# Optimization experiments

Measured on AMD Instinct MI355X. Metric: run time of the kernel, lower is better.

Reference implementation:

```python
import jax, jax.numpy as jnp
import numpy as np

IN_F = 4096
OUT_F = 4096
RANK = 16
ALPHA = 16
SCALING = ALPHA / RANK  # 1.0


def setup_inputs() -> dict:
    key = jax.random.key(0)
    k_x, k_w, k_b, k_a = jax.random.split(key, 4)
    x = jax.random.normal(k_x, (4, 2048, IN_F), dtype=jnp.float32)
    # frozen base linear params
    W = jax.random.normal(k_w, (OUT_F, IN_F), dtype=jnp.float32) * (1.0 / np.sqrt(IN_F))
    b = jax.random.normal(k_b, (OUT_F,), dtype=jnp.float32) * 0.01
    # LoRA params: A kaiming-uniform-like, B zeros per initial_weights(); use small
    bound = np.sqrt(6.0 / IN_F)  # kaiming_uniform(a=sqrt(5)) bound approx
    lora_A = jax.random.uniform(k_a, (RANK, IN_F), dtype=jnp.float32, minval=-bound, maxval=bound)
    lora_B = jax.random.normal(jax.random.fold_in(key, 7), (OUT_F, RANK), dtype=jnp.float32) * 0.01
    lora_bias = jnp.zeros((OUT_F,), dtype=jnp.float32)
    return {"x": x, "W": W, "b": b, "lora_A": lora_A, "lora_B": lora_B, "lora_bias": lora_bias}


def reference(x, W, b, lora_A, lora_B, lora_bias):
    # Original: F.linear(x, W + scaling*B@A, bias=b + lora_bias); dropout is Identity (p=0).
    # Algebraically equivalent form avoiding the [out,in] delta materialization:
    # y = x@W^T + scaling * (x@A^T)@B^T + (b + lora_bias)
    base = jnp.einsum('bsi,oi->bso', x, W)
    low = jnp.einsum('bsr,or->bso', jnp.einsum('bsi,ri->bsr', x, lora_A), lora_B)
    return base + SCALING * low + (b + lora_bias)
```

## Files before the change

kernel.cpp:

```cpp
#include <hip/hip_runtime.h>
#include <hip/hip_bf16.h>
#include <stdint.h>


#define M_DIM 8192
#define N_DIM 4096
#define K_DIM 4096
#define NT    (K_DIM / 64)

typedef __attribute__((ext_vector_type(8))) short bf16x8;
typedef __attribute__((ext_vector_type(4))) float f32x4;

#define BARRIER() __builtin_amdgcn_s_barrier()
#define WAITV8() asm volatile("s_waitcnt vmcnt(8)" ::: "memory")
#define WAITV4() asm volatile("s_waitcnt vmcnt(4)" ::: "memory")
#define WAITV0() asm volatile("s_waitcnt vmcnt(0)" ::: "memory")

static __device__ __forceinline__ unsigned short f2bf(float f) {
    unsigned int u = __builtin_bit_cast(unsigned int, f);
    unsigned int r = (u + 0x7fffu + ((u >> 16) & 1u)) >> 16;
    return (unsigned short)r;
}

__global__ __launch_bounds__(256) void conv_x_kernel(
    const float* __restrict__ x, unsigned short* __restrict__ xb) {
    size_t i = ((size_t)blockIdx.x * 256 + threadIdx.x) * 8;
    float4 a = *(const float4*)(x + i);
    float4 c = *(const float4*)(x + i + 4);
    union { unsigned short us[8]; uint4 v; } u;
    u.us[0] = f2bf(a.x); u.us[1] = f2bf(a.y); u.us[2] = f2bf(a.z); u.us[3] = f2bf(a.w);
    u.us[4] = f2bf(c.x); u.us[5] = f2bf(c.y); u.us[6] = f2bf(c.z); u.us[7] = f2bf(c.w);
    *(uint4*)(xb + i) = u.v;
}

__global__ __launch_bounds__(512) void conv_w_kernel(
    const float* __restrict__ W, const float* __restrict__ lA,
    const float* __restrict__ lB, unsigned short* __restrict__ Wb) {
    const int nb = blockIdx.x * 4;
    const int k0 = threadIdx.x * 8;

    float acc[4][8];
#pragma unroll
    for (int r = 0; r < 4; ++r) {
        const float4* w4 = (const float4*)(W + (size_t)(nb + r) * K_DIM + k0);
        float4 v0 = w4[0], v1 = w4[1];
        acc[r][0] = v0.x; acc[r][1] = v0.y; acc[r][2] = v0.z; acc[r][3] = v0.w;
        acc[r][4] = v1.x; acc[r][5] = v1.y; acc[r][6] = v1.z; acc[r][7] = v1.w;
    }
    float brs[4][16];
#pragma unroll
    for (int r = 0; r < 4; ++r)
#pragma unroll
        for (int t = 0; t < 16; ++t) brs[r][t] = lB[(size_t)(nb + r) * 16 + t];

#pragma unroll
    for (int t = 0; t < 16; ++t) {
        const float4* a4 = (const float4*)(lA + (size_t)t * K_DIM + k0);
        float4 v0 = a4[0], v1 = a4[1];
        float av[8] = {v0.x, v0.y, v0.z, v0.w, v1.x, v1.y, v1.z, v1.w};
#pragma unroll
        for (int r = 0; r < 4; ++r)
#pragma unroll
            for (int j = 0; j < 8; ++j) acc[r][j] += brs[r][t] * av[j];
    }
#pragma unroll
    for (int r = 0; r < 4; ++r) {
        union { unsigned short us[8]; uint4 v; } u;
#pragma unroll
        for (int j = 0; j < 8; ++j) u.us[j] = f2bf(acc[r][j]);
        *(uint4*)(Wb + (size_t)(nb + r) * K_DIM + k0) = u.v;
    }
}

__global__ __launch_bounds__(512, 2) void gemm_kernel(
    const unsigned short* __restrict__ A,
    const unsigned short* __restrict__ B,
    const float* __restrict__ bvec, const float* __restrict__ lbvec,
    float* __restrict__ C) {
    const int tid = threadIdx.x;
    const int lane = tid & 63;
    const int wid = tid >> 6;
    const int wr = wid >> 2;
    const int wc = wid & 3;

    const int bid = blockIdx.x;
    const int ntile = (bid & 7) * 2 + ((bid >> 3) & 1);
    const int mtile = bid >> 4;
    const int m0 = mtile * 256, n0 = ntile * 256;

    __shared__ __align__(16) unsigned short ldsA[2 * 2 * 128 * 64];
    __shared__ __align__(16) unsigned short ldsB[2 * 2 * 128 * 64];

    const int lr8 = lane >> 3;
    const int cch = (lane & 7) ^ lr8;
    const unsigned short* aSb = A + (size_t)(m0 + lr8) * K_DIM + cch * 8;
    const unsigned short* bSb = B + (size_t)(n0 + lr8) * K_DIM + cch * 8;

    auto stageA = [&](int par_, int h, int kt) {
#pragma unroll
        for (int s = 0; s < 2; ++s) {
            const int j = wid * 2 + s;
            const unsigned short* g = aSb + (size_t)(h * 128 + j * 8) * K_DIM + kt * 64;
            __builtin_amdgcn_global_load_lds(
                (const __attribute__((address_space(1))) void*)g,
                (__attribute__((address_space(3))) void*)(ldsA + (par_ * 2 + h) * 8192 + j * 512),
                16, 0, 0);
        }
    };
    auto stageB = [&](int par_, int h, int kt) {
#pragma unroll
        for (int s = 0; s < 2; ++s) {
            const int j = wid * 2 + s;
            const unsigned short* g = bSb + (size_t)(h * 128 + j * 8) * K_DIM + kt * 64;
            __builtin_amdgcn_global_load_lds(
                (const __attribute__((address_space(1))) void*)g,
                (__attribute__((address_space(3))) void*)(ldsB + (par_ * 2 + h) * 8192 + j * 512),
                16, 0, 0);
        }
    };

    const int rowByte = (lane & 15) * 128;
    const int swz = (lane & 7) << 4;
    const int kc0 = (0 * 64 + (lane >> 4) * 16) ^ swz;
    const int kc1 = (1 * 64 + (lane >> 4) * 16) ^ swz;
    const int baseBoff = (wc & 1) * 4096;

    auto readA = [&](int par_, int mf, int kk) -> bf16x8 {
        const char* p = (const char*)(ldsA + (par_ * 2 + wr) * 8192 + mf * 1024) +
                        rowByte + (kk ? kc1 : kc0);
        return *(const bf16x8*)p;
    };
    auto readB = [&](int par_, int nf, int kk) -> bf16x8 {
        const char* p = (const char*)(ldsB + (par_ * 2 + (wc >> 1)) * 8192 + baseBoff + nf * 1024) +
                        rowByte + (kk ? kc1 : kc0);
        return *(const bf16x8*)p;
    };

    f32x4 acc[8][4] = {};
    bf16x8 a[4][2], b[4][2];

    auto mfmaQ = [&](int qm, int qn) {
#pragma unroll
        for (int i = 0; i < 4; ++i)
#pragma unroll
            for (int jn = 0; jn < 2; ++jn)
#pragma unroll
                for (int kk = 0; kk < 2; ++kk)
                    acc[qm * 4 + i][qn * 2 + jn] = __builtin_amdgcn_mfma_f32_16x16x32_bf16(
                        a[i][kk], b[qn * 2 + jn][kk], acc[qm * 4 + i][qn * 2 + jn], 0, 0, 0);
    };

    stageB(0, 0, 0); stageB(0, 1, 0); stageA(0, 0, 0); stageA(0, 1, 0);
    stageB(1, 0, 1); stageB(1, 1, 1); stageA(1, 0, 1); stageA(1, 1, 1);
    WAITV8();
    BARRIER();
#pragma unroll
    for (int nf = 0; nf < 2; ++nf)
#pragma unroll
        for (int kk = 0; kk < 2; ++kk) b[nf][kk] = readB(0, nf, kk);

#define KTILE(kt, par)                                                          \
    {                                                                           \
                         \
        _Pragma("unroll") for (int i = 0; i < 4; ++i)                           \
            _Pragma("unroll") for (int kk = 0; kk < 2; ++kk)                    \
                a[i][kk] = readA(par, i, kk);                                    \
        BARRIER();                                                              \
        __builtin_amdgcn_s_setprio(1); mfmaQ(0, 0); __builtin_amdgcn_s_setprio(0); \
        BARRIER();                                                              \
                                                \
        _Pragma("unroll") for (int nf = 2; nf < 4; ++nf)                        \
            _Pragma("unroll") for (int kk = 0; kk < 2; ++kk)                    \
                b[nf][kk] = readB(par, nf, kk);                                  \
        BARRIER();                                                              \
        __builtin_amdgcn_s_setprio(1); mfmaQ(0, 1); __builtin_amdgcn_s_setprio(0); \
        BARRIER();                                                              \
                                             \
        _Pragma("unroll") for (int i = 0; i < 4; ++i)                           \
            _Pragma("unroll") for (int kk = 0; kk < 2; ++kk)                    \
                a[i][kk] = readA(par, 4 + i, kk);                                \
        if ((kt) + 2 < NT) { stageB(par, 0, (kt) + 2); stageB(par, 1, (kt) + 2); WAITV4(); } \
        else { WAITV0(); }                                                      \
        BARRIER();                                                              \
        __builtin_amdgcn_s_setprio(1); mfmaQ(1, 0); __builtin_amdgcn_s_setprio(0); \
        BARRIER();                                                              \
         \
        if ((kt) + 2 < NT) { stageA(par, 0, (kt) + 2); stageA(par, 1, (kt) + 2); } \
        if ((kt) + 1 < NT) {                                                    \
            _Pragma("unroll") for (int nf = 0; nf < 2; ++nf)                    \
                _Pragma("unroll") for (int kk = 0; kk < 2; ++kk)                \
                    b[nf][kk] = readB((par) ^ 1, nf, kk);                        \
        }                                                                       \
        BARRIER();                                                              \
        __builtin_amdgcn_s_setprio(1); mfmaQ(1, 1); __builtin_amdgcn_s_setprio(0); \
        BARRIER();                                                              \
    }

#pragma unroll 1
    for (int kt = 0; kt < NT; kt += 2) {
        KTILE(kt, 0);
        KTILE(kt + 1, 1);
    }
#undef KTILE

#pragma unroll
    for (int nf = 0; nf < 4; ++nf) {
        const int gc = n0 + wc * 64 + nf * 16 + (lane & 15);
        const float bv = bvec[gc] + lbvec[gc];
#pragma unroll
        for (int mf = 0; mf < 8; ++mf) {
            const int gr0 = m0 + wr * 128 + mf * 16 + (lane >> 4) * 4;
            f32x4 v = acc[mf][nf];
#pragma unroll
            for (int j = 0; j < 4; ++j)
                __builtin_nontemporal_store(v[j] + bv, &C[(size_t)(gr0 + j) * N_DIM + gc]);
        }
    }
}

__global__ __launch_bounds__(256) void naive_kernel(
    const float* __restrict__ x, const float* __restrict__ W,
    const float* __restrict__ b, const float* __restrict__ lA,
    const float* __restrict__ lB, const float* __restrict__ lb,
    float* __restrict__ out) {
    __shared__ float xs[K_DIM];
    __shared__ float ts[16];
    const int m = blockIdx.x;
    const int tid = threadIdx.x;
    for (int k = tid; k < K_DIM; k += 256) xs[k] = x[(size_t)m * K_DIM + k];
    if (tid < 16) ts[tid] = 0.f;
    __syncthreads();
    float part[16] = {};
    for (int k = tid * 16; k < tid * 16 + 16; ++k) {
        float xv = xs[k];
#pragma unroll
        for (int r = 0; r < 16; ++r) part[r] += xv * lA[(size_t)r * K_DIM + k];
    }
#pragma unroll
    for (int r = 0; r < 16; ++r) atomicAdd(&ts[r], part[r]);
    __syncthreads();
    const int n = blockIdx.y * 256 + tid;
    float acc = b[n] + lb[n];
#pragma unroll
    for (int r = 0; r < 16; ++r) acc += ts[r] * lB[(size_t)n * 16 + r];
    const float* wrow = W + (size_t)n * K_DIM;
    for (int k = 0; k < K_DIM; ++k) acc += xs[k] * wrow[k];
    out[(size_t)m * N_DIM + n] = acc;
}

extern "C" void kernel_launch(void* const* d_in, const int* in_sizes, int n_in,
                              void* d_out, int out_size, void* d_ws, size_t ws_size,
                              hipStream_t stream) {
    const float* x  = (const float*)d_in[0];
    const float* W  = (const float*)d_in[1];
    const float* b  = (const float*)d_in[2];
    const float* lA = (const float*)d_in[3];
    const float* lB = (const float*)d_in[4];
    const float* lb = (const float*)d_in[5];
    float* out = (float*)d_out;

    const size_t xb_bytes = (size_t)M_DIM * K_DIM * 2;
    const size_t wb_bytes = (size_t)N_DIM * K_DIM * 2;

    if (ws_size >= xb_bytes + wb_bytes) {
        unsigned short* xb = (unsigned short*)d_ws;
        unsigned short* wb = (unsigned short*)((char*)d_ws + xb_bytes);

        conv_x_kernel<<<(M_DIM * K_DIM) / (256 * 8), 256, 0, stream>>>(x, xb);
        conv_w_kernel<<<N_DIM / 4, 512, 0, stream>>>(W, lA, lB, wb);

        gemm_kernel<<<(M_DIM / 256) * (N_DIM / 256), 512, 0, stream>>>(xb, wb, b, lb, out);
    } else {
        dim3 grid(M_DIM, N_DIM / 256);
        naive_kernel<<<grid, 256, 0, stream>>>(x, W, b, lA, lB, lb, out);
    }
}
```

Measured before the change: 322.3 us.

## Restructure GEMM k-tile loop to k-major MFMA order with fewer barriers

```diff
diff --git a/kernel.cpp b/kernel.cpp
--- a/kernel.cpp
+++ b/kernel.cpp
@@ -13,7 +13,6 @@
 
 #define BARRIER() __builtin_amdgcn_s_barrier()
 #define WAITV8() asm volatile("s_waitcnt vmcnt(8)" ::: "memory")
-#define WAITV4() asm volatile("s_waitcnt vmcnt(4)" ::: "memory")
 #define WAITV0() asm volatile("s_waitcnt vmcnt(0)" ::: "memory")
 
 static __device__ __forceinline__ unsigned short f2bf(float f) {
@@ -137,62 +136,51 @@
     };
 
     f32x4 acc[8][4] = {};
-    bf16x8 a[4][2], b[4][2];
-
-    auto mfmaQ = [&](int qm, int qn) {
-#pragma unroll
-        for (int i = 0; i < 4; ++i)
-#pragma unroll
-            for (int jn = 0; jn < 2; ++jn)
-#pragma unroll
-                for (int kk = 0; kk < 2; ++kk)
-                    acc[qm * 4 + i][qn * 2 + jn] = __builtin_amdgcn_mfma_f32_16x16x32_bf16(
-                        a[i][kk], b[qn * 2 + jn][kk], acc[qm * 4 + i][qn * 2 + jn], 0, 0, 0);
-    };
+    bf16x8 A_[4], B0_[4], B1_[4];
 
     stageB(0, 0, 0); stageB(0, 1, 0); stageA(0, 0, 0); stageA(0, 1, 0);
     stageB(1, 0, 1); stageB(1, 1, 1); stageA(1, 0, 1); stageA(1, 1, 1);
     WAITV8();
     BARRIER();
-#pragma unroll
-    for (int nf = 0; nf < 2; ++nf)
-#pragma unroll
-        for (int kk = 0; kk < 2; ++kk) b[nf][kk] = readB(0, nf, kk);
 
 #define KTILE(kt, par)                                                          \
     {                                                                           \
-                         \
-        _Pragma("unroll") for (int i = 0; i < 4; ++i)                           \
-            _Pragma("unroll") for (int kk = 0; kk < 2; ++kk)                    \
-                a[i][kk] = readA(par, i, kk);                                    \
+        _Pragma("unroll") for (int i = 0; i < 4; ++i) A_[i] = readA(par, i, 0); \
+        _Pragma("unroll") for (int j = 0; j < 4; ++j) B0_[j] = readB(par, j, 0);\
+        _Pragma("unroll") for (int j = 0; j < 4; ++j) B1_[j] = readB(par, j, 1);\
+        __builtin_amdgcn_s_setprio(1);                                          \
+        _Pragma("unroll") for (int i = 0; i < 4; ++i)                           \
+            _Pragma("unroll") for (int j = 0; j < 4; ++j)                       \
+                acc[i][j] = __builtin_amdgcn_mfma_f32_16x16x32_bf16(            \
+                    A_[i], B0_[j], acc[i][j], 0, 0, 0);                         \
+        __builtin_amdgcn_s_setprio(0);                                          \
+        _Pragma("unroll") for (int i = 0; i < 4; ++i) A_[i] = readA(par, 4 + i, 0); \
+        __builtin_amdgcn_s_setprio(1);                                          \
+        _Pragma("unroll") for (int i = 0; i < 4; ++i)                           \
+            _Pragma("unroll") for (int j = 0; j < 4; ++j)                       \
+                acc[4 + i][j] = __builtin_amdgcn_mfma_f32_16x16x32_bf16(        \
+                    A_[i], B0_[j], acc[4 + i][j], 0, 0, 0);                     \
+        __builtin_amdgcn_s_setprio(0);                                          \
+        _Pragma("unroll") for (int i = 0; i < 4; ++i) A_[i] = readA(par, i, 1); \
+        __builtin_amdgcn_s_setprio(1);                                          \
+        _Pragma("unroll") for (int i = 0; i < 4; ++i)                           \
+            _Pragma("unroll") for (int j = 0; j < 4; ++j)                       \
+                acc[i][j] = __builtin_amdgcn_mfma_f32_16x16x32_bf16(            \
+                    A_[i], B1_[j], acc[i][j], 0, 0, 0);                         \
+        __builtin_amdgcn_s_setprio(0);                                          \
+        _Pragma("unroll") for (int i = 0; i < 4; ++i) A_[i] = readA(par, 4 + i, 1); \
+        __builtin_amdgcn_s_setprio(1);                                          \
+        _Pragma("unroll") for (int i = 0; i < 4; ++i)                           \
+            _Pragma("unroll") for (int j = 0; j < 4; ++j)                       \
+                acc[4 + i][j] = __builtin_amdgcn_mfma_f32_16x16x32_bf16(        \
+                    A_[i], B1_[j], acc[4 + i][j], 0, 0, 0);                     \
+        __builtin_amdgcn_s_setprio(0);                                          \
         BARRIER();                                                              \
-        __builtin_amdgcn_s_setprio(1); mfmaQ(0, 0); __builtin_amdgcn_s_setprio(0); \
-        BARRIER();                                                              \
-                                                \
-        _Pragma("unroll") for (int nf = 2; nf < 4; ++nf)                        \
-            _Pragma("unroll") for (int kk = 0; kk < 2; ++kk)                    \
-                b[nf][kk] = readB(par, nf, kk);                                  \
-        BARRIER();                                                              \
-        __builtin_amdgcn_s_setprio(1); mfmaQ(0, 1); __builtin_amdgcn_s_setprio(0); \
-        BARRIER();                                                              \
-                                             \
-        _Pragma("unroll") for (int i = 0; i < 4; ++i)                           \
-            _Pragma("unroll") for (int kk = 0; kk < 2; ++kk)                    \
-                a[i][kk] = readA(par, 4 + i, kk);                                \
-        if ((kt) + 2 < NT) { stageB(par, 0, (kt) + 2); stageB(par, 1, (kt) + 2); WAITV4(); } \
-        else { WAITV0(); }                                                      \
-        BARRIER();                                                              \
-        __builtin_amdgcn_s_setprio(1); mfmaQ(1, 0); __builtin_amdgcn_s_setprio(0); \
-        BARRIER();                                                              \
-         \
-        if ((kt) + 2 < NT) { stageA(par, 0, (kt) + 2); stageA(par, 1, (kt) + 2); } \
-        if ((kt) + 1 < NT) {                                                    \
-            _Pragma("unroll") for (int nf = 0; nf < 2; ++nf)                    \
-                _Pragma("unroll") for (int kk = 0; kk < 2; ++kk)                \
-                    b[nf][kk] = readB((par) ^ 1, nf, kk);                        \
-        }                                                                       \
-        BARRIER();                                                              \
-        __builtin_amdgcn_s_setprio(1); mfmaQ(1, 1); __builtin_amdgcn_s_setprio(0); \
+        if ((kt) + 2 < NT) {                                                    \
+            stageB(par, 0, (kt) + 2); stageB(par, 1, (kt) + 2);                 \
+            stageA(par, 0, (kt) + 2); stageA(par, 1, (kt) + 2);                 \
+            WAITV8();                                                           \
+        } else { WAITV0(); }                                                    \
         BARRIER();                                                              \
     }
 
```

New measurement: 330.2 us. +2.5%, slower.

## Restructure GEMM to 4 waves with 128x128 warp tiles and k-half register double-buffering

Applied to the files above, without the earlier changes.

```diff
diff --git a/kernel.cpp b/kernel.cpp
--- a/kernel.cpp
+++ b/kernel.cpp
@@ -12,9 +12,11 @@
 typedef __attribute__((ext_vector_type(4))) float f32x4;
 
 #define BARRIER() __builtin_amdgcn_s_barrier()
-#define WAITV8() asm volatile("s_waitcnt vmcnt(8)" ::: "memory")
-#define WAITV4() asm volatile("s_waitcnt vmcnt(4)" ::: "memory")
-#define WAITV0() asm volatile("s_waitcnt vmcnt(0)" ::: "memory")
+#define WAITV16() asm volatile("s_waitcnt vmcnt(16)" ::: "memory")
+#define WAITV0()  asm volatile("s_waitcnt vmcnt(0)" ::: "memory")
+#define LGKM0()   do { asm volatile("s_waitcnt lgkmcnt(0)" ::: "memory"); \
+                       __builtin_amdgcn_sched_barrier(0); } while (0)
+#define SCHED_FENCE() __builtin_amdgcn_sched_barrier(0)
 
 static __device__ __forceinline__ unsigned short f2bf(float f) {
     unsigned int u = __builtin_bit_cast(unsigned int, f);
@@ -72,7 +74,7 @@
     }
 }
 
-__global__ __launch_bounds__(512, 2) void gemm_kernel(
+__global__ __launch_bounds__(256, 1) void gemm_kernel(
     const unsigned short* __restrict__ A,
     const unsigned short* __restrict__ B,
     const float* __restrict__ bvec, const float* __restrict__ lbvec,
@@ -80,8 +82,8 @@
     const int tid = threadIdx.x;
     const int lane = tid & 63;
     const int wid = tid >> 6;
-    const int wr = wid >> 2;
-    const int wc = wid & 3;
+    const int wr = wid >> 1;
+    const int wc = wid & 1;
 
     const int bid = blockIdx.x;
     const int ntile = (bid & 7) * 2 + ((bid >> 3) & 1);
@@ -98,8 +100,8 @@
 
     auto stageA = [&](int par_, int h, int kt) {
 #pragma unroll
-        for (int s = 0; s < 2; ++s) {
-            const int j = wid * 2 + s;
+        for (int s = 0; s < 4; ++s) {
+            const int j = wid * 4 + s;
             const unsigned short* g = aSb + (size_t)(h * 128 + j * 8) * K_DIM + kt * 64;
             __builtin_amdgcn_global_load_lds(
                 (const __attribute__((address_space(1))) void*)g,
@@ -109,8 +111,8 @@
     };
     auto stageB = [&](int par_, int h, int kt) {
 #pragma unroll
-        for (int s = 0; s < 2; ++s) {
-            const int j = wid * 2 + s;
+        for (int s = 0; s < 4; ++s) {
+            const int j = wid * 4 + s;
             const unsigned short* g = bSb + (size_t)(h * 128 + j * 8) * K_DIM + kt * 64;
             __builtin_amdgcn_global_load_lds(
                 (const __attribute__((address_space(1))) void*)g,
@@ -118,12 +120,15 @@
                 16, 0, 0);
         }
     };
+    auto stageTile = [&](int par_, int kt) {
+        stageB(par_, 0, kt); stageB(par_, 1, kt);
+        stageA(par_, 0, kt); stageA(par_, 1, kt);
+    };
 
     const int rowByte = (lane & 15) * 128;
     const int swz = (lane & 7) << 4;
     const int kc0 = (0 * 64 + (lane >> 4) * 16) ^ swz;
     const int kc1 = (1 * 64 + (lane >> 4) * 16) ^ swz;
-    const int baseBoff = (wc & 1) * 4096;
 
     auto readA = [&](int par_, int mf, int kk) -> bf16x8 {
         const char* p = (const char*)(ldsA + (par_ * 2 + wr) * 8192 + mf * 1024) +
@@ -131,81 +136,72 @@
         return *(const bf16x8*)p;
     };
     auto readB = [&](int par_, int nf, int kk) -> bf16x8 {
-        const char* p = (const char*)(ldsB + (par_ * 2 + (wc >> 1)) * 8192 + baseBoff + nf * 1024) +
+        const char* p = (const char*)(ldsB + (par_ * 2 + wc) * 8192 + nf * 1024) +
                         rowByte + (kk ? kc1 : kc0);
         return *(const bf16x8*)p;
     };
 
-    f32x4 acc[8][4] = {};
-    bf16x8 a[4][2], b[4][2];
-
-    auto mfmaQ = [&](int qm, int qn) {
-#pragma unroll
-        for (int i = 0; i < 4; ++i)
-#pragma unroll
-            for (int jn = 0; jn < 2; ++jn)
-#pragma unroll
-                for (int kk = 0; kk < 2; ++kk)
-                    acc[qm * 4 + i][qn * 2 + jn] = __builtin_amdgcn_mfma_f32_16x16x32_bf16(
-                        a[i][kk], b[qn * 2 + jn][kk], acc[qm * 4 + i][qn * 2 + jn], 0, 0, 0);
-    };
-
-    stageB(0, 0, 0); stageB(0, 1, 0); stageA(0, 0, 0); stageA(0, 1, 0);
-    stageB(1, 0, 1); stageB(1, 1, 1); stageA(1, 0, 1); stageA(1, 1, 1);
-    WAITV8();
+    f32x4 acc[8][8] = {};
+    bf16x8 A0[8], B0[8], A1[8], B1[8];
+
+    stageTile(0, 0);
+    stageTile(1, 1);
+    WAITV16();
     BARRIER();
 #pragma unroll
-    for (int nf = 0; nf < 2; ++nf)
-#pragma unroll
-        for (int kk = 0; kk < 2; ++kk) b[nf][kk] = readB(0, nf, kk);
-
-#define KTILE(kt, par)                                                          \
-    {                                                                           \
-                         \
-        _Pragma("unroll") for (int i = 0; i < 4; ++i)                           \
-            _Pragma("unroll") for (int kk = 0; kk < 2; ++kk)                    \
-                a[i][kk] = readA(par, i, kk);                                    \
-        BARRIER();                                                              \
-        __builtin_amdgcn_s_setprio(1); mfmaQ(0, 0); __builtin_amdgcn_s_setprio(0); \
-        BARRIER();                                                              \
-                                                \
-        _Pragma("unroll") for (int nf = 2; nf < 4; ++nf)                        \
-            _Pragma("unroll") for (int kk = 0; kk < 2; ++kk)                    \
-                b[nf][kk] = readB(par, nf, kk);                                  \
-        BARRIER();                                                              \
-        __builtin_amdgcn_s_setprio(1); mfmaQ(0, 1); __builtin_amdgcn_s_setprio(0); \
-        BARRIER();                                                              \
-                                             \
-        _Pragma("unroll") for (int i = 0; i < 4; ++i)                           \
-            _Pragma("unroll") for (int kk = 0; kk < 2; ++kk)                    \
-                a[i][kk] = readA(par, 4 + i, kk);                                \
-        if ((kt) + 2 < NT) { stageB(par, 0, (kt) + 2); stageB(par, 1, (kt) + 2); WAITV4(); } \
-        else { WAITV0(); }                                                      \
-        BARRIER();                                                              \
-        __builtin_amdgcn_s_setprio(1); mfmaQ(1, 0); __builtin_amdgcn_s_setprio(0); \
-        BARRIER();                                                              \
-         \
-        if ((kt) + 2 < NT) { stageA(par, 0, (kt) + 2); stageA(par, 1, (kt) + 2); } \
-        if ((kt) + 1 < NT) {                                                    \
-            _Pragma("unroll") for (int nf = 0; nf < 2; ++nf)                    \
-                _Pragma("unroll") for (int kk = 0; kk < 2; ++kk)                \
-                    b[nf][kk] = readB((par) ^ 1, nf, kk);                        \
-        }                                                                       \
-        BARRIER();                                                              \
-        __builtin_amdgcn_s_setprio(1); mfmaQ(1, 1); __builtin_amdgcn_s_setprio(0); \
-        BARRIER();                                                              \
-    }
+    for (int mf = 0; mf < 8; ++mf) A0[mf] = readA(0, mf, 0);
+#pragma unroll
+    for (int nf = 0; nf < 8; ++nf) B0[nf] = readB(0, nf, 0);
+    LGKM0();
+#pragma unroll
+    for (int mf = 0; mf < 8; ++mf) A1[mf] = readA(0, mf, 1);
+#pragma unroll
+    for (int nf = 0; nf < 8; ++nf) B1[nf] = readB(0, nf, 1);
+    SCHED_FENCE();
 
 #pragma unroll 1
-    for (int kt = 0; kt < NT; kt += 2) {
-        KTILE(kt, 0);
-        KTILE(kt + 1, 1);
-    }
-#undef KTILE
-
-#pragma unroll
-    for (int nf = 0; nf < 4; ++nf) {
-        const int gc = n0 + wc * 64 + nf * 16 + (lane & 15);
+    for (int kt = 0; kt < NT; ++kt) {
+        const int par = kt & 1;
+        __builtin_amdgcn_s_setprio(1);
+#pragma unroll
+        for (int i = 0; i < 8; ++i)
+#pragma unroll
+            for (int j = 0; j < 8; ++j)
+                acc[i][j] = __builtin_amdgcn_mfma_f32_16x16x32_bf16(
+                    A0[i], B0[j], acc[i][j], 0, 0, 0);
+        __builtin_amdgcn_s_setprio(0);
+        LGKM0();
+        WAITV0();
+        BARRIER();
+        if (kt + 2 < NT) stageTile(par, kt + 2);
+        if (kt + 1 < NT) {
+#pragma unroll
+            for (int mf = 0; mf < 8; ++mf) A0[mf] = readA(par ^ 1, mf, 0);
+#pragma unroll
+            for (int nf = 0; nf < 8; ++nf) B0[nf] = readB(par ^ 1, nf, 0);
+        }
+        SCHED_FENCE();
+        __builtin_amdgcn_s_setprio(1);
+#pragma unroll
+        for (int i = 0; i < 8; ++i)
+#pragma unroll
+            for (int j = 0; j < 8; ++j)
+                acc[i][j] = __builtin_amdgcn_mfma_f32_16x16x32_bf16(
+                    A1[i], B1[j], acc[i][j], 0, 0, 0);
+        __builtin_amdgcn_s_setprio(0);
+        LGKM0();
+        if (kt + 1 < NT) {
+#pragma unroll
+            for (int mf = 0; mf < 8; ++mf) A1[mf] = readA(par ^ 1, mf, 1);
+#pragma unroll
+            for (int nf = 0; nf < 8; ++nf) B1[nf] = readB(par ^ 1, nf, 1);
+        }
+        SCHED_FENCE();
+    }
+
+#pragma unroll
+    for (int nf = 0; nf < 8; ++nf) {
+        const int gc = n0 + wc * 128 + nf * 16 + (lane & 15);
         const float bv = bvec[gc] + lbvec[gc];
 #pragma unroll
         for (int mf = 0; mf < 8; ++mf) {
@@ -269,7 +265,7 @@
         conv_x_kernel<<<(M_DIM * K_DIM) / (256 * 8), 256, 0, stream>>>(x, xb);
         conv_w_kernel<<<N_DIM / 4, 512, 0, stream>>>(W, lA, lB, wb);
 
-        gemm_kernel<<<(M_DIM / 256) * (N_DIM / 256), 512, 0, stream>>>(xb, wb, b, lb, out);
+        gemm_kernel<<<(M_DIM / 256) * (N_DIM / 256), 256, 0, stream>>>(xb, wb, b, lb, out);
     } else {
         dim3 grid(M_DIM, N_DIM / 256);
         naive_kernel<<<grid, 256, 0, stream>>>(x, W, b, lA, lB, lb, out);
```

Measured after the change: 1.047 ms. +224.8%, slower.
